# Kernel optimization log

Hardware: AMD Instinct MI355X
Metric: run time of the kernel (lower is better)

Reference implementation:

```python
import jax, jax.numpy as jnp
import numpy as np

N_NODES = 50000
N_EDGES = 1600000
EMB_DIM = 128
N_PATH = 2
N_LAYERS = 2
N_HEADS = 8
HEAD_DIM = EMB_DIM // N_HEADS


def setup_inputs() -> dict:
    key = jax.random.key(0)
    ks = jax.random.split(key, 6)
    fs = jax.random.normal(ks[0], (N_PATH, N_NODES, EMB_DIM), dtype=jnp.float32)
    W = jax.random.normal(ks[1], (N_PATH, N_LAYERS, EMB_DIM, EMB_DIM), dtype=jnp.float32) * (1.0 / np.sqrt(EMB_DIM))
    attn_l = jax.random.normal(ks[2], (N_PATH, N_LAYERS, N_HEADS, HEAD_DIM), dtype=jnp.float32) * 0.1
    attn_r = jax.random.normal(ks[3], (N_PATH, N_LAYERS, N_HEADS, HEAD_DIM), dtype=jnp.float32) * 0.1
    bias = jnp.zeros((N_PATH, N_LAYERS, EMB_DIM), dtype=jnp.float32)
    edges = jax.random.randint(ks[4], (N_PATH, 2, N_EDGES), 0, N_NODES, dtype=jnp.int32)
    return {"fs": fs, "W": W, "attn_l": attn_l, "attn_r": attn_r, "bias": bias, "edges": edges}


def gat_conv(h, src, dst, W, al, ar, b):
    # h: [N, F_in]; DGL GATConv, eval mode (dropout off), residual Identity, bias, ELU.
    N = h.shape[0]
    H, D = al.shape
    feat = (h @ W).reshape(N, H, D)                      # fc projection
    el = jnp.einsum('nhd,hd->nh', feat, al)              # [N, H]
    er = jnp.einsum('nhd,hd->nh', feat, ar)              # [N, H]
    e = jax.nn.leaky_relu(el[src] + er[dst], 0.2)        # [E, H]
    # edge softmax over incoming edges of each destination node
    emax = jax.ops.segment_max(e, dst, num_segments=N)   # [N, H], -inf for 0-in-degree
    emax = jnp.where(jnp.isfinite(emax), emax, 0.0)
    ex = jnp.exp(e - emax[dst])                          # [E, H]
    esum = jax.ops.segment_sum(ex, dst, num_segments=N)  # [N, H]
    alpha = ex / jnp.maximum(esum[dst], 1e-9)            # [E, H]
    msg = alpha[:, :, None] * feat[src]                  # [E, H, D]
    rst = jax.ops.segment_sum(msg, dst, num_segments=N)  # [N, H, D]
    rst = rst + h.reshape(N, H, D) + b.reshape(1, H, D)  # residual (Identity) + bias
    out = jax.nn.elu(rst)
    return out.reshape(N, H * D), alpha


def reference(fs, W, attn_l, attn_r, bias, edges):
    semantic_embeddings = []
    element_weights = []
    for p in range(N_PATH):
        h = fs[p]
        src, dst = edges[p, 0], edges[p, 1]
        attn = None
        for l in range(N_LAYERS):
            h, attn = gat_conv(h, src, dst, W[p, l], attn_l[p, l], attn_r[p, l], bias[p, l])
        semantic_embeddings.append(h)
        element_weights.append(attn)
    return jnp.stack(semantic_embeddings), jnp.stack(element_weights)
```

## Files before the change

### kernel.cpp

```cpp
#include <hip/hip_runtime.h>
#include <hip/hip_bf16.h>

#define NND 50000
#define NE  1600000
#define EMB 128
#define NH  8
#define HD  16
#define NB  98

typedef __attribute__((ext_vector_type(8))) short short8v;
typedef __attribute__((ext_vector_type(4))) float f32x4;

__device__ __forceinline__ float lrelu(float x) { return x > 0.f ? x : 0.2f * x; }
__device__ __forceinline__ float elu(float x)   { return x > 0.f ? x : expm1f(x); }

__device__ __forceinline__ unsigned short f2bf(float x) {
    __hip_bfloat16 b = __float2bfloat16(x);
    return *reinterpret_cast<unsigned short*>(&b);
}
__device__ __forceinline__ float bf2f(unsigned short u) {
    __hip_bfloat16 b = *reinterpret_cast<__hip_bfloat16*>(&u);
    return __bfloat162float(b);
}

__global__ __launch_bounds__(256) void hsplit(
    const float* __restrict__ hin, unsigned short* __restrict__ hhi, unsigned short* __restrict__ hlo)
{
    int idx = blockIdx.x * 256 + threadIdx.x;
    const float4* h4 = reinterpret_cast<const float4*>(hin);
    float4 v0 = h4[(size_t)idx * 2];
    float4 v1 = h4[(size_t)idx * 2 + 1];
    float xs[8] = { v0.x, v0.y, v0.z, v0.w, v1.x, v1.y, v1.z, v1.w };
    unsigned short hi[8], lo[8];
    #pragma unroll
    for (int j = 0; j < 8; ++j) {
        hi[j] = f2bf(xs[j]);
        lo[j] = f2bf(xs[j] - bf2f(hi[j]));
    }
    *reinterpret_cast<uint4*>(hhi + (size_t)idx * 8) = *reinterpret_cast<uint4*>(hi);
    *reinterpret_cast<uint4*>(hlo + (size_t)idx * 8) = *reinterpret_cast<uint4*>(lo);
}

__global__ __launch_bounds__(256) void wpack(
    const float* __restrict__ Wm, unsigned short* __restrict__ bphi, unsigned short* __restrict__ bplo)
{
    int s = blockIdx.x * 256 + threadIdx.x;
    if (s >= 2048) return;
    int n    = s >> 8;
    int kt   = (s >> 6) & 3;
    int lane = s & 63;
    int col  = n * 16 + (lane & 15);
    int krow = kt * 32 + ((lane >> 4) << 3);
    #pragma unroll
    for (int j = 0; j < 8; ++j) {
        float x = Wm[(size_t)(krow + j) * EMB + col];
        unsigned short hi = f2bf(x);
        unsigned short lo = f2bf(x - bf2f(hi));
        bphi[(size_t)s * 8 + j] = hi;
        bplo[(size_t)s * 8 + j] = lo;
    }
}

__global__ __launch_bounds__(256) void mfma_gemm(
    const unsigned short* __restrict__ hhi, const unsigned short* __restrict__ hlo,
    const unsigned short* __restrict__ bphi, const unsigned short* __restrict__ bplo,
    const float* __restrict__ alv, const float* __restrict__ arv,
    unsigned short* __restrict__ feat_bf, float* __restrict__ el, float* __restrict__ er)
{
    const int lane = threadIdx.x & 63;
    const int wave = threadIdx.x >> 6;
    const int rowbase = blockIdx.x * 16;

    f32x4 acc[2];
    acc[0] = (f32x4){0.f, 0.f, 0.f, 0.f};
    acc[1] = (f32x4){0.f, 0.f, 0.f, 0.f};

    const int ar  = rowbase + (lane & 15);
    const int car = ar < NND ? ar : NND - 1;
    const int kofs = (lane >> 4) * 8;

    #pragma unroll
    for (int kt = 0; kt < 4; ++kt) {
        const int k0 = kt * 32 + kofs;
        short8v ah = *reinterpret_cast<const short8v*>(hhi + (size_t)car * EMB + k0);
        short8v av = *reinterpret_cast<const short8v*>(hlo + (size_t)car * EMB + k0);
        #pragma unroll
        for (int q = 0; q < 2; ++q) {
            const int nn = wave * 2 + q;
            const size_t bofs = ((size_t)(nn * 4 + kt) * 64 + lane) * 8;
            short8v bh = *reinterpret_cast<const short8v*>(bphi + bofs);
            short8v bl = *reinterpret_cast<const short8v*>(bplo + bofs);
            acc[q] = __builtin_amdgcn_mfma_f32_16x16x32_bf16(ah, bh, acc[q], 0, 0, 0);
            acc[q] = __builtin_amdgcn_mfma_f32_16x16x32_bf16(av, bh, acc[q], 0, 0, 0);
            acc[q] = __builtin_amdgcn_mfma_f32_16x16x32_bf16(ah, bl, acc[q], 0, 0, 0);
        }
    }

    const int colr = lane & 15;
    const int rgrp = lane >> 4;
    const int row0 = rowbase + rgrp * 4;
    #pragma unroll
    for (int q = 0; q < 2; ++q) {
        const int nn = wave * 2 + q;
        f32x4 a = acc[q];
        #pragma unroll
        for (int r = 0; r < 4; ++r) {
            if (row0 + r < NND)
                feat_bf[(size_t)(row0 + r) * EMB + nn * 16 + colr] = f2bf(a[r]);
        }
        const float alc = alv[nn * 16 + colr];
        const float arc = arv[nn * 16 + colr];
        float pl[4], pr[4];
        #pragma unroll
        for (int r = 0; r < 4; ++r) { pl[r] = a[r] * alc; pr[r] = a[r] * arc; }
        #pragma unroll
        for (int mask = 1; mask < 16; mask <<= 1) {
            #pragma unroll
            for (int r = 0; r < 4; ++r) {
                pl[r] += __shfl_xor(pl[r], mask);
                pr[r] += __shfl_xor(pr[r], mask);
            }
        }
        if (colr == 0) {
            #pragma unroll
            for (int r = 0; r < 4; ++r) {
                int row = row0 + r;
                if (row < NND) {
                    el[row * NH + nn] = pl[r];
                    er[row * NH + nn] = pr[r];
                }
            }
        }
    }
}

__global__ __launch_bounds__(256) void bucket_count(
    const int* __restrict__ dst, int* __restrict__ bcnt)
{
    __shared__ int hist[NB];
    const int t = threadIdx.x;
    for (int b = t; b < NB; b += 256) hist[b] = 0;
    __syncthreads();
    const int e0 = blockIdx.x * 2048 + t * 8;
    #pragma unroll
    for (int j = 0; j < 8; ++j) {
        int e = e0 + j;
        if (e < NE) atomicAdd(&hist[dst[e] >> 9], 1);
    }
    __syncthreads();
    for (int b = t; b < NB; b += 256)
        if (hist[b]) atomicAdd(&bcnt[b], hist[b]);
}

__global__ __launch_bounds__(128) void scan_bucket(
    const int* __restrict__ bcnt, int* __restrict__ bbase, int* __restrict__ bcur)
{
    __shared__ int s[128];
    const int t = threadIdx.x;
    s[t] = (t < NB) ? bcnt[t] : 0;
    __syncthreads();
    for (int off = 1; off < 128; off <<= 1) {
        int v = (t >= off) ? s[t - off] : 0;
        __syncthreads();
        s[t] += v;
        __syncthreads();
    }
    int excl = (t > 0) ? s[t - 1] : 0;
    if (t <= NB) bbase[t] = excl;
    if (t < NB)  bcur[t]  = excl;
}

__global__ __launch_bounds__(256) void bucket_scatter(
    const int* __restrict__ src, const int* __restrict__ dst,
    int* __restrict__ bcur, int* __restrict__ ebuf)
{
    __shared__ int hist[NB];
    __shared__ int base[NB];
    __shared__ int lcur[NB];
    const int t  = threadIdx.x;
    const int e0 = blockIdx.x * 2048 + t * 8;

    for (int b = t; b < NB; b += 256) { hist[b] = 0; lcur[b] = 0; }
    __syncthreads();

    int sj[8], dj[8];
    bool vj[8];
    #pragma unroll
    for (int j = 0; j < 8; ++j) {
        int e = e0 + j;
        vj[j] = (e < NE);
        if (vj[j]) {
            sj[j] = src[e];
            dj[j] = dst[e];
            atomicAdd(&hist[dj[j] >> 9], 1);
        }
    }
    __syncthreads();
    for (int b = t; b < NB; b += 256) {
        int c = hist[b];
        base[b] = c > 0 ? atomicAdd(&bcur[b], c) : 0;
    }
    __syncthreads();
    #pragma unroll
    for (int j = 0; j < 8; ++j) {
        if (vj[j]) {
            int b   = dj[j] >> 9;
            int off = atomicAdd(&lcur[b], 1);
            ebuf[(size_t)base[b] + off] = (sj[j] << 9) | (dj[j] & 511);
        }
    }
}

__global__ __launch_bounds__(1024) void bucket_fill(
    const int* __restrict__ bbase, const int* __restrict__ ebuf,
    int* __restrict__ rowptr, int* __restrict__ csrsrc)
{
    __shared__ int hist[512];
    __shared__ int excl[512];
    const int b    = blockIdx.x;
    const int n0   = b << 9;
    const int t    = threadIdx.x;
    const int base = bbase[b];
    const int cnt  = bbase[b + 1] - base;

    if (t < 512) hist[t] = 0;
    __syncthreads();
    for (int i = t; i < cnt; i += 1024)
        atomicAdd(&hist[ebuf[base + i] & 511], 1);
    __syncthreads();
    if (t < 512) excl[t] = hist[t];
    __syncthreads();
    for (int off = 1; off < 512; off <<= 1) {
        int v = 0;
        if (t < 512 && t >= off) v = excl[t - off];
        __syncthreads();
        if (t < 512) excl[t] += v;
        __syncthreads();
    }
    if (t < 512) {
        int e = excl[t] - hist[t];
        int n = n0 + t;
        if (n < NND) rowptr[n] = base + e;
        hist[t] = e;
    }
    if (b == NB - 1 && t == 0) rowptr[NND] = NE;
    __syncthreads();
    for (int i = t; i < cnt; i += 1024) {
        int ed = ebuf[base + i];
        int p = atomicAdd(&hist[ed & 511], 1);
        csrsrc[base + p] = ed >> 9;
    }
}

__global__ __launch_bounds__(256) void gather_agg(
    const int* __restrict__ rowptr, const int* __restrict__ csrsrc,
    const float* __restrict__ el, const float* __restrict__ er,
    const unsigned int* __restrict__ featu,
    const float* __restrict__ hin_f32,
    const unsigned int* __restrict__ hin_hi,
    const unsigned int* __restrict__ hin_lo,
    const float* __restrict__ bias,
    float* __restrict__ esum_out,
    float* __restrict__ hout_f32,
    unsigned int* __restrict__ hhi_out,
    unsigned int* __restrict__ hlo_out)
{
    const int wid  = (blockIdx.x * blockDim.x + threadIdx.x) >> 6;
    const int lane = threadIdx.x & 63;
    if (wid >= NND) return;
    const int n = wid;
    const int h = lane >> 3;

    const float ern = er[n * NH + h];
    const int r0 = __builtin_amdgcn_readfirstlane(rowptr[n]);
    const int r1 = __builtin_amdgcn_readfirstlane(rowptr[n + 1]);

    float acc0 = 0.f, acc1 = 0.f, es = 0.f;

    int i = r0;
    for (; i + 16 <= r1; i += 16) {
        int sj[16];
        #pragma unroll
        for (int j = 0; j < 16; ++j) sj[j] = csrsrc[i + j];
        unsigned int vs[16];
        #pragma unroll
        for (int j = 0; j < 16; ++j) vs[j] = featu[(size_t)sj[j] * 64 + lane];
        float w[16];
        #pragma unroll
        for (int j = 0; j < 16; ++j) w[j] = __expf(lrelu(el[sj[j] * NH + h] + ern));
        #pragma unroll
        for (int j = 0; j < 16; ++j) {
            es  += w[j];
            acc0 = fmaf(w[j], __uint_as_float(vs[j] << 16), acc0);
            acc1 = fmaf(w[j], __uint_as_float(vs[j] & 0xffff0000u), acc1);
        }
    }
    if (i + 8 <= r1) {
        int sj[8];
        #pragma unroll
        for (int j = 0; j < 8; ++j) sj[j] = csrsrc[i + j];
        unsigned int vs[8];
        #pragma unroll
        for (int j = 0; j < 8; ++j) vs[j] = featu[(size_t)sj[j] * 64 + lane];
        #pragma unroll
        for (int j = 0; j < 8; ++j) {
            float w = __expf(lrelu(el[sj[j] * NH + h] + ern));
            es  += w;
            acc0 = fmaf(w, __uint_as_float(vs[j] << 16), acc0);
            acc1 = fmaf(w, __uint_as_float(vs[j] & 0xffff0000u), acc1);
        }
        i += 8;
    }
    for (; i < r1; ++i) {
        int sj = csrsrc[i];
        unsigned int v = featu[(size_t)sj * 64 + lane];
        float w = __expf(lrelu(el[sj * NH + h] + ern));
        es  += w;
        acc0 = fmaf(w, __uint_as_float(v << 16), acc0);
        acc1 = fmaf(w, __uint_as_float(v & 0xffff0000u), acc1);
    }

    if ((lane & 7) == 0) esum_out[n * NH + h] = es;
    const float inv = 1.f / fmaxf(es, 1e-9f);

    float h0, h1;
    if (hin_f32) {
        float2 hv = reinterpret_cast<const float2*>(hin_f32)[(size_t)n * 64 + lane];
        h0 = hv.x; h1 = hv.y;
    } else {
        unsigned int hiu = hin_hi[(size_t)n * 64 + lane];
        unsigned int lou = hin_lo[(size_t)n * 64 + lane];
        h0 = __uint_as_float(hiu << 16) + __uint_as_float(lou << 16);
        h1 = __uint_as_float(hiu & 0xffff0000u) + __uint_as_float(lou & 0xffff0000u);
    }
    float o0 = elu(fmaf(acc0, inv, h0 + bias[lane * 2]));
    float o1 = elu(fmaf(acc1, inv, h1 + bias[lane * 2 + 1]));

    if (hout_f32) {
        reinterpret_cast<float2*>(hout_f32)[(size_t)n * 64 + lane] = make_float2(o0, o1);
    } else {
        unsigned short hi0 = f2bf(o0), hi1 = f2bf(o1);
        unsigned short lo0 = f2bf(o0 - bf2f(hi0)), lo1 = f2bf(o1 - bf2f(hi1));
        hhi_out[(size_t)n * 64 + lane] = (unsigned int)hi0 | ((unsigned int)hi1 << 16);
        hlo_out[(size_t)n * 64 + lane] = (unsigned int)lo0 | ((unsigned int)lo1 << 16);
    }
}

__global__ __launch_bounds__(256) void alpha_write(
    const int* __restrict__ src, const int* __restrict__ dst,
    const float* __restrict__ el, const float* __restrict__ er,
    const float* __restrict__ esum, float* __restrict__ aout)
{
    int tid = blockIdx.x * blockDim.x + threadIdx.x;
    if (tid >= NE * NH) return;
    int e = tid >> 3;
    int h = tid & 7;
    int s = src[e], d = dst[e];
    float x = lrelu(el[s * NH + h] + er[d * NH + h]);
    float a = __expf(x) / fmaxf(esum[d * NH + h], 1e-9f);
    aout[(size_t)e * NH + h] = a;
}

extern "C" void kernel_launch(void* const* d_in, const int* in_sizes, int n_in,
                              void* d_out, int out_size, void* d_ws, size_t ws_size,
                              hipStream_t stream) {
    const float* fs   = (const float*)d_in[0];
    const float* W    = (const float*)d_in[1];
    const float* al   = (const float*)d_in[2];
    const float* ar   = (const float*)d_in[3];
    const float* bias = (const float*)d_in[4];
    const int*   edges= (const int*)d_in[5];

    float* out       = (float*)d_out;
    float* out_emb   = out;
    float* out_alpha = out + (size_t)2 * NND * EMB;

    char* ws = (char*)d_ws;
    unsigned short* feat_bf = (unsigned short*)ws; ws += (size_t)NND * EMB * 2;
    unsigned short* hhi     = (unsigned short*)ws; ws += (size_t)NND * EMB * 2;
    unsigned short* hlo     = (unsigned short*)ws; ws += (size_t)NND * EMB * 2;
    float*          el      = (float*)ws;          ws += (size_t)NND * NH * 4;
    float*          er      = (float*)ws;          ws += (size_t)NND * NH * 4;
    float*          esum    = (float*)ws;          ws += (size_t)NND * NH * 4;
    int*            rowptr  = (int*)ws;            ws += (size_t)(NND + 1) * 4;
    int*            bcnt    = (int*)ws;            ws += (size_t)128 * 4;
    int*            bbase   = (int*)ws;            ws += (size_t)132 * 4;
    int*            bcur    = (int*)ws;            ws += (size_t)128 * 4;
    int*            csrsrc  = (int*)ws;            ws += (size_t)NE * 4;
    int*            ebuf    = (int*)ws;            ws += (size_t)NE * 4;
    unsigned short* bphi    = (unsigned short*)ws; ws += (size_t)16384 * 2;
    unsigned short* bplo    = (unsigned short*)ws; ws += (size_t)16384 * 2;

    unsigned int* featu = (unsigned int*)feat_bf;
    unsigned int* hhi_u = (unsigned int*)hhi;
    unsigned int* hlo_u = (unsigned int*)hlo;

    for (int p = 0; p < 2; ++p) {
        const int* src = edges + (size_t)p * 2 * NE;
        const int* dst = src + NE;

        hipMemsetAsync(bcnt, 0, (size_t)128 * 4, stream);
        bucket_count<<<(NE + 2047) / 2048, 256, 0, stream>>>(dst, bcnt);
        scan_bucket<<<1, 128, 0, stream>>>(bcnt, bbase, bcur);
        bucket_scatter<<<(NE + 2047) / 2048, 256, 0, stream>>>(src, dst, bcur, ebuf);
        bucket_fill<<<NB, 1024, 0, stream>>>(bbase, ebuf, rowptr, csrsrc);

        for (int l = 0; l < 2; ++l) {
            const float* fsp  = fs + (size_t)p * NND * EMB;
            const float* Wl   = W    + (size_t)(p * 2 + l) * EMB * EMB;
            const float* alv  = al   + (size_t)(p * 2 + l) * NH * HD;
            const float* arv  = ar   + (size_t)(p * 2 + l) * NH * HD;
            const float* bl   = bias + (size_t)(p * 2 + l) * EMB;

            wpack<<<8, 256, 0, stream>>>(Wl, bphi, bplo);
            if (l == 0)
                hsplit<<<NND * EMB / 8 / 256, 256, 0, stream>>>(fsp, hhi, hlo);

            mfma_gemm<<<(NND + 15) / 16, 256, 0, stream>>>(hhi, hlo, bphi, bplo, alv, arv, feat_bf, el, er);

            if (l == 0) {
                gather_agg<<<(NND + 3) / 4, 256, 0, stream>>>(
                    rowptr, csrsrc, el, er, featu,
                    fsp, nullptr, nullptr, bl, esum,
                    nullptr, hhi_u, hlo_u);
            } else {
                gather_agg<<<(NND + 3) / 4, 256, 0, stream>>>(
                    rowptr, csrsrc, el, er, featu,
                    nullptr, hhi_u, hlo_u, bl, esum,
                    out_emb + (size_t)p * NND * EMB, nullptr, nullptr);
                alpha_write<<<((size_t)NE * NH + 255) / 256, 256, 0, stream>>>(
                    src, dst, el, er, esum, out_alpha + (size_t)p * NE * NH);
            }
        }
    }
}
```

Measured before the change: 667.0 us.

## Batch CSR build and weight packing across paths, fuse hsplit into GEMM, vectorize alpha

The CSR bucket-sort kernels now handle both paths in one launch through a grid y-dimension, and all four weight matrices are packed in a single launch up front. This removes per-path launches and serialization. The hsplit pass is folded into the first-layer GEMM, which reads fp32 and splits it into hi/lo bf16 in registers, and ebuf now reuses the hlo buffer. alpha_write processes one edge per thread with float4 loads and stores, using fast exp and divide, which may shift numerics slightly.

```diff
diff --git a/kernel.cpp b/kernel.cpp
--- a/kernel.cpp
+++ b/kernel.cpp
@@ -23,34 +23,18 @@
     return __bfloat162float(b);
 }
 
-__global__ __launch_bounds__(256) void hsplit(
-    const float* __restrict__ hin, unsigned short* __restrict__ hhi, unsigned short* __restrict__ hlo)
-{
-    int idx = blockIdx.x * 256 + threadIdx.x;
-    const float4* h4 = reinterpret_cast<const float4*>(hin);
-    float4 v0 = h4[(size_t)idx * 2];
-    float4 v1 = h4[(size_t)idx * 2 + 1];
-    float xs[8] = { v0.x, v0.y, v0.z, v0.w, v1.x, v1.y, v1.z, v1.w };
-    unsigned short hi[8], lo[8];
-    #pragma unroll
-    for (int j = 0; j < 8; ++j) {
-        hi[j] = f2bf(xs[j]);
-        lo[j] = f2bf(xs[j] - bf2f(hi[j]));
-    }
-    *reinterpret_cast<uint4*>(hhi + (size_t)idx * 8) = *reinterpret_cast<uint4*>(hi);
-    *reinterpret_cast<uint4*>(hlo + (size_t)idx * 8) = *reinterpret_cast<uint4*>(lo);
-}
-
-__global__ __launch_bounds__(256) void wpack(
-    const float* __restrict__ Wm, unsigned short* __restrict__ bphi, unsigned short* __restrict__ bplo)
+__global__ __launch_bounds__(256) void wpack4(
+    const float* __restrict__ W, unsigned short* __restrict__ bphi, unsigned short* __restrict__ bplo)
 {
     int s = blockIdx.x * 256 + threadIdx.x;
-    if (s >= 2048) return;
-    int n    = s >> 8;
-    int kt   = (s >> 6) & 3;
-    int lane = s & 63;
+    int q    = s >> 11;
+    int sidx = s & 2047;
+    int n    = sidx >> 8;
+    int kt   = (sidx >> 6) & 3;
+    int lane = sidx & 63;
     int col  = n * 16 + (lane & 15);
     int krow = kt * 32 + ((lane >> 4) << 3);
+    const float* Wm = W + (size_t)q * EMB * EMB;
     #pragma unroll
     for (int j = 0; j < 8; ++j) {
         float x = Wm[(size_t)(krow + j) * EMB + col];
@@ -61,8 +45,8 @@
     }
 }
 
-__global__ __launch_bounds__(256) void mfma_gemm(
-    const unsigned short* __restrict__ hhi, const unsigned short* __restrict__ hlo,
+__global__ __launch_bounds__(256) void mfma_gemm_f32(
+    const float* __restrict__ hin,
     const unsigned short* __restrict__ bphi, const unsigned short* __restrict__ bplo,
     const float* __restrict__ alv, const float* __restrict__ arv,
     unsigned short* __restrict__ feat_bf, float* __restrict__ el, float* __restrict__ er)
@@ -82,8 +66,16 @@
     #pragma unroll
     for (int kt = 0; kt < 4; ++kt) {
         const int k0 = kt * 32 + kofs;
-        short8v ah = *reinterpret_cast<const short8v*>(hhi + (size_t)car * EMB + k0);
-        short8v av = *reinterpret_cast<const short8v*>(hlo + (size_t)car * EMB + k0);
+        const float4* fr = reinterpret_cast<const float4*>(hin + (size_t)car * EMB + k0);
+        float4 x0 = fr[0], x1 = fr[1];
+        float xs[8] = { x0.x, x0.y, x0.z, x0.w, x1.x, x1.y, x1.z, x1.w };
+        short8v ah, av;
+        #pragma unroll
+        for (int j = 0; j < 8; ++j) {
+            unsigned short hi = f2bf(xs[j]);
+            ah[j] = (short)hi;
+            av[j] = (short)f2bf(xs[j] - bf2f(hi));
+        }
         #pragma unroll
         for (int q = 0; q < 2; ++q) {
             const int nn = wave * 2 + q;
@@ -134,9 +126,84 @@
     }
 }
 
+__global__ __launch_bounds__(256) void mfma_gemm_bf(
+    const unsigned short* __restrict__ hhi, const unsigned short* __restrict__ hlo,
+    const unsigned short* __restrict__ bphi, const unsigned short* __restrict__ bplo,
+    const float* __restrict__ alv, const float* __restrict__ arv,
+    unsigned short* __restrict__ feat_bf, float* __restrict__ el, float* __restrict__ er)
+{
+    const int lane = threadIdx.x & 63;
+    const int wave = threadIdx.x >> 6;
+    const int rowbase = blockIdx.x * 16;
+
+    f32x4 acc[2];
+    acc[0] = (f32x4){0.f, 0.f, 0.f, 0.f};
+    acc[1] = (f32x4){0.f, 0.f, 0.f, 0.f};
+
+    const int ar  = rowbase + (lane & 15);
+    const int car = ar < NND ? ar : NND - 1;
+    const int kofs = (lane >> 4) * 8;
+
+    #pragma unroll
+    for (int kt = 0; kt < 4; ++kt) {
+        const int k0 = kt * 32 + kofs;
+        short8v ah = *reinterpret_cast<const short8v*>(hhi + (size_t)car * EMB + k0);
+        short8v av = *reinterpret_cast<const short8v*>(hlo + (size_t)car * EMB + k0);
+        #pragma unroll
+        for (int q = 0; q < 2; ++q) {
+            const int nn = wave * 2 + q;
+            const size_t bofs = ((size_t)(nn * 4 + kt) * 64 + lane) * 8;
+            short8v bh = *reinterpret_cast<const short8v*>(bphi + bofs);
+            short8v bl = *reinterpret_cast<const short8v*>(bplo + bofs);
+            acc[q] = __builtin_amdgcn_mfma_f32_16x16x32_bf16(ah, bh, acc[q], 0, 0, 0);
+            acc[q] = __builtin_amdgcn_mfma_f32_16x16x32_bf16(av, bh, acc[q], 0, 0, 0);
+            acc[q] = __builtin_amdgcn_mfma_f32_16x16x32_bf16(ah, bl, acc[q], 0, 0, 0);
+        }
+    }
+
+    const int colr = lane & 15;
+    const int rgrp = lane >> 4;
+    const int row0 = rowbase + rgrp * 4;
+    #pragma unroll
+    for (int q = 0; q < 2; ++q) {
+        const int nn = wave * 2 + q;
+        f32x4 a = acc[q];
+        #pragma unroll
+        for (int r = 0; r < 4; ++r) {
+            if (row0 + r < NND)
+                feat_bf[(size_t)(row0 + r) * EMB + nn * 16 + colr] = f2bf(a[r]);
+        }
+        const float alc = alv[nn * 16 + colr];
+        const float arc = arv[nn * 16 + colr];
+        float pl[4], pr[4];
+        #pragma unroll
+        for (int r = 0; r < 4; ++r) { pl[r] = a[r] * alc; pr[r] = a[r] * arc; }
+        #pragma unroll
+        for (int mask = 1; mask < 16; mask <<= 1) {
+            #pragma unroll
+            for (int r = 0; r < 4; ++r) {
+                pl[r] += __shfl_xor(pl[r], mask);
+                pr[r] += __shfl_xor(pr[r], mask);
+            }
+        }
+        if (colr == 0) {
+            #pragma unroll
+            for (int r = 0; r < 4; ++r) {
+                int row = row0 + r;
+                if (row < NND) {
+                    el[row * NH + nn] = pl[r];
+                    er[row * NH + nn] = pr[r];
+                }
+            }
+        }
+    }
+}
+
 __global__ __launch_bounds__(256) void bucket_count(
-    const int* __restrict__ dst, int* __restrict__ bcnt)
-{
+    const int* __restrict__ edges, int* __restrict__ bcnt)
+{
+    const int p = blockIdx.y;
+    const int* dst = edges + (size_t)p * 2 * NE + NE;
     __shared__ int hist[NB];
     const int t = threadIdx.x;
     for (int b = t; b < NB; b += 256) hist[b] = 0;
@@ -149,15 +216,16 @@
     }
     __syncthreads();
     for (int b = t; b < NB; b += 256)
-        if (hist[b]) atomicAdd(&bcnt[b], hist[b]);
+        if (hist[b]) atomicAdd(&bcnt[p * 128 + b], hist[b]);
 }
 
 __global__ __launch_bounds__(128) void scan_bucket(
     const int* __restrict__ bcnt, int* __restrict__ bbase, int* __restrict__ bcur)
 {
+    const int p = blockIdx.x;
     __shared__ int s[128];
     const int t = threadIdx.x;
-    s[t] = (t < NB) ? bcnt[t] : 0;
+    s[t] = (t < NB) ? bcnt[p * 128 + t] : 0;
     __syncthreads();
     for (int off = 1; off < 128; off <<= 1) {
         int v = (t >= off) ? s[t - off] : 0;
@@ -166,14 +234,17 @@
         __syncthreads();
     }
     int excl = (t > 0) ? s[t - 1] : 0;
-    if (t <= NB) bbase[t] = excl;
-    if (t < NB)  bcur[t]  = excl;
+    if (t <= NB) bbase[p * 128 + t] = excl;
+    if (t < NB)  bcur[p * 128 + t]  = excl;
 }
 
 __global__ __launch_bounds__(256) void bucket_scatter(
-    const int* __restrict__ src, const int* __restrict__ dst,
-    int* __restrict__ bcur, int* __restrict__ ebuf)
-{
+    const int* __restrict__ edges, int* __restrict__ bcur, int* __restrict__ ebuf)
+{
+    const int p = blockIdx.y;
+    const int* src = edges + (size_t)p * 2 * NE;
+    const int* dst = src + NE;
+    int* eb = ebuf + (size_t)p * NE;
     __shared__ int hist[NB];
     __shared__ int base[NB];
     __shared__ int lcur[NB];
@@ -198,7 +269,7 @@
     __syncthreads();
     for (int b = t; b < NB; b += 256) {
         int c = hist[b];
-        base[b] = c > 0 ? atomicAdd(&bcur[b], c) : 0;
+        base[b] = c > 0 ? atomicAdd(&bcur[p * 128 + b], c) : 0;
     }
     __syncthreads();
     #pragma unroll
@@ -206,7 +277,7 @@
         if (vj[j]) {
             int b   = dj[j] >> 9;
             int off = atomicAdd(&lcur[b], 1);
-            ebuf[(size_t)base[b] + off] = (sj[j] << 9) | (dj[j] & 511);
+            eb[(size_t)base[b] + off] = (sj[j] << 9) | (dj[j] & 511);
         }
     }
 }
@@ -215,18 +286,22 @@
     const int* __restrict__ bbase, const int* __restrict__ ebuf,
     int* __restrict__ rowptr, int* __restrict__ csrsrc)
 {
+    const int p = blockIdx.y;
+    const int* eb = ebuf + (size_t)p * NE;
+    int* rp = rowptr + (size_t)p * (NND + 1);
+    int* cs = csrsrc + (size_t)p * NE;
     __shared__ int hist[512];
     __shared__ int excl[512];
     const int b    = blockIdx.x;
     const int n0   = b << 9;
     const int t    = threadIdx.x;
-    const int base = bbase[b];
-    const int cnt  = bbase[b + 1] - base;
+    const int base = bbase[p * 128 + b];
+    const int cnt  = bbase[p * 128 + b + 1] - base;
 
     if (t < 512) hist[t] = 0;
     __syncthreads();
     for (int i = t; i < cnt; i += 1024)
-        atomicAdd(&hist[ebuf[base + i] & 511], 1);
+        atomicAdd(&hist[eb[base + i] & 511], 1);
     __syncthreads();
     if (t < 512) excl[t] = hist[t];
     __syncthreads();
@@ -240,15 +315,15 @@
     if (t < 512) {
         int e = excl[t] - hist[t];
         int n = n0 + t;
-        if (n < NND) rowptr[n] = base + e;
+        if (n < NND) rp[n] = base + e;
         hist[t] = e;
     }
-    if (b == NB - 1 && t == 0) rowptr[NND] = NE;
+    if (b == NB - 1 && t == 0) rp[NND] = NE;
     __syncthreads();
     for (int i = t; i < cnt; i += 1024) {
-        int ed = ebuf[base + i];
-        int p = atomicAdd(&hist[ed & 511], 1);
-        csrsrc[base + p] = ed >> 9;
+        int ed = eb[base + i];
+        int q = atomicAdd(&hist[ed & 511], 1);
+        cs[base + q] = ed >> 9;
     }
 }
 
@@ -346,19 +421,32 @@
     }
 }
 
-__global__ __launch_bounds__(256) void alpha_write(
+__global__ __launch_bounds__(256) void alpha_write8(
     const int* __restrict__ src, const int* __restrict__ dst,
     const float* __restrict__ el, const float* __restrict__ er,
     const float* __restrict__ esum, float* __restrict__ aout)
 {
-    int tid = blockIdx.x * blockDim.x + threadIdx.x;
-    if (tid >= NE * NH) return;
-    int e = tid >> 3;
-    int h = tid & 7;
+    int e = blockIdx.x * 256 + threadIdx.x;
+    if (e >= NE) return;
     int s = src[e], d = dst[e];
-    float x = lrelu(el[s * NH + h] + er[d * NH + h]);
-    float a = __expf(x) / fmaxf(esum[d * NH + h], 1e-9f);
-    aout[(size_t)e * NH + h] = a;
+    const float4* el4 = reinterpret_cast<const float4*>(el + (size_t)s * 8);
+    const float4* er4 = reinterpret_cast<const float4*>(er + (size_t)d * 8);
+    const float4* es4 = reinterpret_cast<const float4*>(esum + (size_t)d * 8);
+    float4 L0 = el4[0], L1 = el4[1];
+    float4 R0 = er4[0], R1 = er4[1];
+    float4 S0 = es4[0], S1 = es4[1];
+    float4 a0, a1;
+    a0.x = __fdividef(__expf(lrelu(L0.x + R0.x)), fmaxf(S0.x, 1e-9f));
+    a0.y = __fdividef(__expf(lrelu(L0.y + R0.y)), fmaxf(S0.y, 1e-9f));
+    a0.z = __fdividef(__expf(lrelu(L0.z + R0.z)), fmaxf(S0.z, 1e-9f));
+    a0.w = __fdividef(__expf(lrelu(L0.w + R0.w)), fmaxf(S0.w, 1e-9f));
+    a1.x = __fdividef(__expf(lrelu(L1.x + R1.x)), fmaxf(S1.x, 1e-9f));
+    a1.y = __fdividef(__expf(lrelu(L1.y + R1.y)), fmaxf(S1.y, 1e-9f));
+    a1.z = __fdividef(__expf(lrelu(L1.z + R1.z)), fmaxf(S1.z, 1e-9f));
+    a1.w = __fdividef(__expf(lrelu(L1.w + R1.w)), fmaxf(S1.w, 1e-9f));
+    float4* o4 = reinterpret_cast<float4*>(aout + (size_t)e * 8);
+    o4[0] = a0;
+    o4[1] = a1;
 }
 
 extern "C" void kernel_launch(void* const* d_in, const int* in_sizes, int n_in,
@@ -376,59 +464,68 @@
     float* out_alpha = out + (size_t)2 * NND * EMB;
 
     char* ws = (char*)d_ws;
-    unsigned short* feat_bf = (unsigned short*)ws; ws += (size_t)NND * EMB * 2;
-    unsigned short* hhi     = (unsigned short*)ws; ws += (size_t)NND * EMB * 2;
-    unsigned short* hlo     = (unsigned short*)ws; ws += (size_t)NND * EMB * 2;
-    float*          el      = (float*)ws;          ws += (size_t)NND * NH * 4;
-    float*          er      = (float*)ws;          ws += (size_t)NND * NH * 4;
-    float*          esum    = (float*)ws;          ws += (size_t)NND * NH * 4;
-    int*            rowptr  = (int*)ws;            ws += (size_t)(NND + 1) * 4;
-    int*            bcnt    = (int*)ws;            ws += (size_t)128 * 4;
-    int*            bbase   = (int*)ws;            ws += (size_t)132 * 4;
-    int*            bcur    = (int*)ws;            ws += (size_t)128 * 4;
-    int*            csrsrc  = (int*)ws;            ws += (size_t)NE * 4;
-    int*            ebuf    = (int*)ws;            ws += (size_t)NE * 4;
-    unsigned short* bphi    = (unsigned short*)ws; ws += (size_t)16384 * 2;
-    unsigned short* bplo    = (unsigned short*)ws; ws += (size_t)16384 * 2;
-
+    auto take = [&](size_t bytes) {
+        char* r = ws;
+        ws += (bytes + 15) & ~(size_t)15;
+        return r;
+    };
+    unsigned short* feat_bf = (unsigned short*)take((size_t)NND * EMB * 2);
+    unsigned short* hhi     = (unsigned short*)take((size_t)NND * EMB * 2);
+    unsigned short* hlo     = (unsigned short*)take((size_t)NND * EMB * 2);
+    float*          el      = (float*)take((size_t)NND * NH * 4);
+    float*          er      = (float*)take((size_t)NND * NH * 4);
+    float*          esum    = (float*)take((size_t)NND * NH * 4);
+    int*            rowptr  = (int*)take((size_t)2 * (NND + 1) * 4);
+    int*            bcnt    = (int*)take((size_t)2 * 128 * 4);
+    int*            bbase   = (int*)take((size_t)2 * 128 * 4);
+    int*            bcur    = (int*)take((size_t)2 * 128 * 4);
+    int*            csrsrc  = (int*)take((size_t)2 * NE * 4);
+    unsigned short* bphi    = (unsigned short*)take((size_t)4 * 16384 * 2);
+    unsigned short* bplo    = (unsigned short*)take((size_t)4 * 16384 * 2);
+
+    int*          ebuf  = (int*)hlo;
     unsigned int* featu = (unsigned int*)feat_bf;
     unsigned int* hhi_u = (unsigned int*)hhi;
     unsigned int* hlo_u = (unsigned int*)hlo;
 
+    hipMemsetAsync(bcnt, 0, (size_t)2 * 128 * 4, stream);
+    bucket_count<<<dim3((NE + 2047) / 2048, 2), 256, 0, stream>>>(edges, bcnt);
+    scan_bucket<<<2, 128, 0, stream>>>(bcnt, bbase, bcur);
+    bucket_scatter<<<dim3((NE + 2047) / 2048, 2), 256, 0, stream>>>(edges, bcur, ebuf);
+    bucket_fill<<<dim3(NB, 2), 1024, 0, stream>>>(bbase, ebuf, rowptr, csrsrc);
+
+    wpack4<<<32, 256, 0, stream>>>(W, bphi, bplo);
+
     for (int p = 0; p < 2; ++p) {
-        const int* src = edges + (size_t)p * 2 * NE;
-        const int* dst = src + NE;
-
-        hipMemsetAsync(bcnt, 0, (size_t)128 * 4, stream);
-        bucket_count<<<(NE + 2047) / 2048, 256, 0, stream>>>(dst, bcnt);
-        scan_bucket<<<1, 128, 0, stream>>>(bcnt, bbase, bcur);
-        bucket_scatter<<<(NE + 2047) / 2048, 256, 0, stream>>>(src, dst, bcur, ebuf);
-        bucket_fill<<<NB, 1024, 0, stream>>>(bbase, ebuf, rowptr, csrsrc);
+        const int*   src = edges + (size_t)p * 2 * NE;
+        const int*   dst = src + NE;
+        const int*   rp  = rowptr + (size_t)p * (NND + 1);
+        const int*   cs  = csrsrc + (size_t)p * NE;
+        const float* fsp = fs + (size_t)p * NND * EMB;
 
         for (int l = 0; l < 2; ++l) {
-            const float* fsp  = fs + (size_t)p * NND * EMB;
-            const float* Wl   = W    + (size_t)(p * 2 + l) * EMB * EMB;
-            const float* alv  = al   + (size_t)(p * 2 + l) * NH * HD;
-            const float* arv  = ar   + (size_t)(p * 2 + l) * NH * HD;
-            const float* bl   = bias + (size_t)(p * 2 + l) * EMB;
-
-            wpack<<<8, 256, 0, stream>>>(Wl, bphi, bplo);
-            if (l == 0)
-                hsplit<<<NND * EMB / 8 / 256, 256, 0, stream>>>(fsp, hhi, hlo);
-
-            mfma_gemm<<<(NND + 15) / 16, 256, 0, stream>>>(hhi, hlo, bphi, bplo, alv, arv, feat_bf, el, er);
+            const int q = p * 2 + l;
+            const unsigned short* bphi_q = bphi + (size_t)q * 16384;
+            const unsigned short* bplo_q = bplo + (size_t)q * 16384;
+            const float* alv = al   + (size_t)q * NH * HD;
+            const float* arv = ar   + (size_t)q * NH * HD;
+            const float* bl  = bias + (size_t)q * EMB;
 
             if (l == 0) {
+                mfma_gemm_f32<<<(NND + 15) / 16, 256, 0, stream>>>(
+                    fsp, bphi_q, bplo_q, alv, arv, feat_bf, el, er);
                 gather_agg<<<(NND + 3) / 4, 256, 0, stream>>>(
-                    rowptr, csrsrc, el, er, featu,
+                    rp, cs, el, er, featu,
                     fsp, nullptr, nullptr, bl, esum,
                     nullptr, hhi_u, hlo_u);
             } else {
+                mfma_gemm_bf<<<(NND + 15) / 16, 256, 0, stream>>>(
+                    hhi, hlo, bphi_q, bplo_q, alv, arv, feat_bf, el, er);
                 gather_agg<<<(NND + 3) / 4, 256, 0, stream>>>(
-                    rowptr, csrsrc, el, er, featu,
+                    rp, cs, el, er, featu,
                     nullptr, hhi_u, hlo_u, bl, esum,
                     out_emb + (size_t)p * NND * EMB, nullptr, nullptr);
-                alpha_write<<<((size_t)NE * NH + 255) / 256, 256, 0, stream>>>(
+                alpha_write8<<<(NE + 255) / 256, 256, 0, stream>>>(
                     src, dst, el, er, esum, out_alpha + (size_t)p * NE * NH);
             }
         }
```

After: 598.2 us. -10.3%, faster.
